# Kernel tuning notes

Measured on AMD Instinct MI355X. Metric: run time of the kernel, lower is better.

The kernel has to match this reference:

```python
import jax, jax.numpy as jnp
import numpy as np

EPS = 1e-6

def setup_inputs() -> dict:
    key = jax.random.key(0)
    k1, k2, k3 = jax.random.split(key, 3)
    B, C, H, W = 2048, 256, 7, 7
    base = jax.random.normal(k1, (B, C, H, W), dtype=jnp.float32)
    moment = jax.random.normal(k2, (B, C, H, W), dtype=jnp.float32)
    A_matrix = jax.random.randint(k3, (B, H * W, H * W), 0, 2, dtype=jnp.int32)
    return {"base": base, "moment": moment, "A_matrix": A_matrix}

def reference(base, moment, A_matrix):
    B, C, H, W = base.shape
    P = H * W  # 49
    b = base.reshape(B, C, P)      # (B, C, 49)
    m = moment.reshape(B, C, P)    # (B, C, 49)
    # pairwise dot over channel dim via batched matmul (avoids BxCx49x49 broadcast)
    dots = jnp.einsum('bcp,bcq->bpq', b, m)            # (B, 49, 49)
    nb = jnp.maximum(jnp.linalg.norm(b, axis=1), EPS)  # (B, 49)
    nm = jnp.maximum(jnp.linalg.norm(m, axis=1), EPS)  # (B, 49)
    cos_sim = dots / (nb[:, :, None] * nm[:, None, :])
    mask = A_matrix.astype(bool)
    # masked mean without dynamic-size gather
    num = jnp.sum(jnp.where(mask, cos_sim, 0.0))
    den = jnp.sum(mask).astype(cos_sim.dtype)
    return -(num / den)
```

## Files before the change

### kernel.cpp

```cpp
#include <hip/hip_runtime.h>
#include <hip/hip_bf16.h>
#include <stdint.h>


typedef __attribute__((ext_vector_type(8))) short short8;
typedef __attribute__((ext_vector_type(4))) float floatx4;

#define P 49
#define CP 12544
#define NMASK 2401
#define MT_STRIDE 264
#define WS_STRIDE 72

__device__ __forceinline__ uint16_t f2bf(float x) {
  union { float f; uint32_t u; } v; v.f = x;
  uint32_t r = v.u + 0x7fffu + ((v.u >> 16) & 1u);
  return (uint16_t)(r >> 16);
}
__device__ __forceinline__ float bf2f(uint16_t h) {
  union { uint32_t u; float f; } v; v.u = ((uint32_t)h) << 16; return v.f;
}

__device__ __forceinline__ void stage_T(const float* __restrict__ src,
                                        uint16_t* dstT, float* nred,
                                        int wv, int mrow, int kgrp) {
  float s0[8], s1[8];
  #pragma unroll
  for (int j = 0; j < 8; ++j) { s0[j] = 0.f; s1[j] = 0.f; }

  #pragma unroll
  for (int cti = 0; cti < 2; ++cti) {
    const int c = (2 * wv + cti) * 16 + mrow;
    const float* row = src + c * P;
    float4 a0 = *(const float4*)(row + kgrp * 8);
    float4 a1 = *(const float4*)(row + kgrp * 8 + 4);
    float4 b0, b1;
    if (kgrp < 2) {
      b0 = *(const float4*)(row + 32 + kgrp * 8);
      b1 = *(const float4*)(row + 32 + kgrp * 8 + 4);
    } else if (kgrp == 2) {
      b0 = make_float4(row[48], 0.f, 0.f, 0.f);
      b1 = make_float4(0.f, 0.f, 0.f, 0.f);
    } else {
      b0 = make_float4(0.f, 0.f, 0.f, 0.f);
      b1 = make_float4(0.f, 0.f, 0.f, 0.f);
    }
    s0[0] = fmaf(a0.x, a0.x, s0[0]); s0[1] = fmaf(a0.y, a0.y, s0[1]);
    s0[2] = fmaf(a0.z, a0.z, s0[2]); s0[3] = fmaf(a0.w, a0.w, s0[3]);
    s0[4] = fmaf(a1.x, a1.x, s0[4]); s0[5] = fmaf(a1.y, a1.y, s0[5]);
    s0[6] = fmaf(a1.z, a1.z, s0[6]); s0[7] = fmaf(a1.w, a1.w, s0[7]);
    s1[0] = fmaf(b0.x, b0.x, s1[0]); s1[1] = fmaf(b0.y, b0.y, s1[1]);
    s1[2] = fmaf(b0.z, b0.z, s1[2]); s1[3] = fmaf(b0.w, b0.w, s1[3]);
    s1[4] = fmaf(b1.x, b1.x, s1[4]); s1[5] = fmaf(b1.y, b1.y, s1[5]);
    s1[6] = fmaf(b1.z, b1.z, s1[6]); s1[7] = fmaf(b1.w, b1.w, s1[7]);

    float av[8] = {a0.x, a0.y, a0.z, a0.w, a1.x, a1.y, a1.z, a1.w};
    #pragma unroll
    for (int j = 0; j < 8; ++j)
      dstT[(kgrp * 8 + j) * MT_STRIDE + c] = f2bf(av[j]);
    if (kgrp < 2) {
      float bw[8] = {b0.x, b0.y, b0.z, b0.w, b1.x, b1.y, b1.z, b1.w};
      #pragma unroll
      for (int j = 0; j < 8; ++j)
        dstT[(32 + kgrp * 8 + j) * MT_STRIDE + c] = f2bf(bw[j]);
    } else if (kgrp == 2) {
      dstT[48 * MT_STRIDE + c] = f2bf(b0.x);
    }
  }

  #pragma unroll
  for (int j = 0; j < 8; ++j) {
    s0[j] += __shfl_xor(s0[j], 1); s0[j] += __shfl_xor(s0[j], 2);
    s0[j] += __shfl_xor(s0[j], 4); s0[j] += __shfl_xor(s0[j], 8);
    s1[j] += __shfl_xor(s1[j], 1); s1[j] += __shfl_xor(s1[j], 2);
    s1[j] += __shfl_xor(s1[j], 4); s1[j] += __shfl_xor(s1[j], 8);
  }
  if (mrow == 0) {
    float* nb_ = nred + wv * 64 + kgrp * 8;
    *(float4*)(nb_ + 0)  = make_float4(s0[0], s0[1], s0[2], s0[3]);
    *(float4*)(nb_ + 4)  = make_float4(s0[4], s0[5], s0[6], s0[7]);
    *(float4*)(nb_ + 32) = make_float4(s1[0], s1[1], s1[2], s1[3]);
    *(float4*)(nb_ + 36) = make_float4(s1[4], s1[5], s1[6], s1[7]);
  }
}

__global__ __launch_bounds__(512, 4) void pixpro_main(
    const float* __restrict__ base, const float* __restrict__ moment,
    const int* __restrict__ A, float* __restrict__ ws_num, float* __restrict__ ws_cnt)
{
  __shared__ __align__(16) uint16_t mT[P * MT_STRIDE];
  __shared__ __align__(16) uint16_t bT[P * MT_STRIDE];
  __shared__ __align__(16) float nredM[8 * 64];
  __shared__ __align__(16) float nredB[8 * 64];
  __shared__ __align__(16) uint16_t wS[P * WS_STRIDE];
  __shared__ float numredS[8], cntredS[8];

  const int b    = blockIdx.x;
  const int tid  = threadIdx.x;
  const int lane = tid & 63;
  const int wv   = tid >> 6;
  const int mrow = lane & 15;
  const int kgrp = (lane >> 4) & 3;

  const float* gb = base   + (size_t)b * CP;
  const float* gm = moment + (size_t)b * CP;
  const int*   gA = A      + (size_t)b * NMASK;

  stage_T(gm, mT, nredM, wv, mrow, kgrp);

  const bool btask = tid < P * 8;
  const int  bp    = tid >> 3;
  const int  bqg   = tid & 7;
  const int  bq0   = bqg * 8;
  int bmask[8];
  #pragma unroll
  for (int j = 0; j < 8; ++j) bmask[j] = 0;
  if (btask) {
    const int* Ar = gA + bp * P + bq0;
    if (bqg <= 5) {
      int4 u0 = *(const int4*)(Ar);
      int4 u1 = *(const int4*)(Ar + 4);
      bmask[0] = u0.x; bmask[1] = u0.y; bmask[2] = u0.z; bmask[3] = u0.w;
      bmask[4] = u1.x; bmask[5] = u1.y; bmask[6] = u1.z; bmask[7] = u1.w;
    } else if (bqg == 6) {
      bmask[0] = Ar[0];
    }
  }

  stage_T(gb, bT, nredB, wv, mrow, kgrp);

  __syncthreads();

  int cntpart = 0;
  if (btask) {
    float4 a0 = make_float4(0.f, 0.f, 0.f, 0.f);
    float4 a1 = make_float4(0.f, 0.f, 0.f, 0.f);
    float nb2 = 0.f;
    #pragma unroll
    for (int w = 0; w < 8; ++w) {
      const float* nr = &nredM[w * 64 + bq0];
      float4 u0 = *(const float4*)(nr);
      float4 u1 = *(const float4*)(nr + 4);
      a0.x += u0.x; a0.y += u0.y; a0.z += u0.z; a0.w += u0.w;
      a1.x += u1.x; a1.y += u1.y; a1.z += u1.z; a1.w += u1.w;
      nb2 += nredB[w * 64 + bp];
    }
    const float inb = 1.0f / fmaxf(sqrtf(nb2), 1e-6f);
    float wf[8];
    wf[0] = bmask[0] ? inb * (1.0f / fmaxf(sqrtf(a0.x), 1e-6f)) : 0.f;
    wf[1] = bmask[1] ? inb * (1.0f / fmaxf(sqrtf(a0.y), 1e-6f)) : 0.f;
    wf[2] = bmask[2] ? inb * (1.0f / fmaxf(sqrtf(a0.z), 1e-6f)) : 0.f;
    wf[3] = bmask[3] ? inb * (1.0f / fmaxf(sqrtf(a0.w), 1e-6f)) : 0.f;
    wf[4] = bmask[4] ? inb * (1.0f / fmaxf(sqrtf(a1.x), 1e-6f)) : 0.f;
    wf[5] = bmask[5] ? inb * (1.0f / fmaxf(sqrtf(a1.y), 1e-6f)) : 0.f;
    wf[6] = bmask[6] ? inb * (1.0f / fmaxf(sqrtf(a1.z), 1e-6f)) : 0.f;
    wf[7] = bmask[7] ? inb * (1.0f / fmaxf(sqrtf(a1.w), 1e-6f)) : 0.f;
    #pragma unroll
    for (int j = 0; j < 8; ++j) cntpart += bmask[j];
    short8 w8;
    #pragma unroll
    for (int j = 0; j < 8; ++j) w8[j] = (short)f2bf(wf[j]);
    *(short8*)&wS[bp * WS_STRIDE + bq0] = w8;
  }

  const int pt  = wv & 3;
  const int qt1i = 2 * (wv >> 2) + 1;
  const int pbaseV  = (pt < 3) ? pt * 16 : 33;
  const int qbase0  = (qt1i - 1) * 16;
  const int qbase1  = (qt1i < 3) ? qt1i * 16 : 33;

  const int arow  = (pbaseV + mrow) * MT_STRIDE;
  const int brow0 = (qbase0 + mrow) * MT_STRIDE;
  const int brow1 = (qbase1 + mrow) * MT_STRIDE;

  floatx4 acc0 = (floatx4){0.f, 0.f, 0.f, 0.f};
  floatx4 acc1 = (floatx4){0.f, 0.f, 0.f, 0.f};
  #pragma unroll
  for (int ks = 0; ks < 8; ++ks) {
    const int off = ks * 32 + kgrp * 8;
    short8 af  = *(const short8*)&bT[arow  + off];
    short8 bf0 = *(const short8*)&mT[brow0 + off];
    short8 bf1 = *(const short8*)&mT[brow1 + off];
    acc0 = __builtin_amdgcn_mfma_f32_16x16x32_bf16(af, bf0, acc0, 0, 0, 0);
    acc1 = __builtin_amdgcn_mfma_f32_16x16x32_bf16(af, bf1, acc1, 0, 0, 0);
  }

  __syncthreads();

  const bool vq1 = (qt1i < 3) || (mrow == 15);
  const int  q0r = qbase0 + mrow;
  const int  q1r = qbase1 + mrow;
  float numpart = 0.f;
  #pragma unroll
  for (int r = 0; r < 4; ++r) {
    const int rr = kgrp * 4 + r;
    const int p  = pbaseV + rr;
    const bool vp = (pt < 3) || (rr == 15);
    if (vp) {
      float w0 = bf2f(wS[p * WS_STRIDE + q0r]);
      float w1 = vq1 ? bf2f(wS[p * WS_STRIDE + q1r]) : 0.f;
      numpart = fmaf(w0, acc0[r], numpart);
      numpart = fmaf(w1, acc1[r], numpart);
    }
  }

  float cntf = (float)cntpart;
  #pragma unroll
  for (int off = 32; off > 0; off >>= 1) {
    numpart += __shfl_xor(numpart, off);
    cntf    += __shfl_xor(cntf, off);
  }
  if (lane == 0) { numredS[wv] = numpart; cntredS[wv] = cntf; }
  __syncthreads();

  if (tid < 64) {
    float n = (tid < 8) ? numredS[tid] : 0.f;
    float c = (tid < 8) ? cntredS[tid] : 0.f;
    #pragma unroll
    for (int off = 4; off > 0; off >>= 1) {
      n += __shfl_xor(n, off);
      c += __shfl_xor(c, off);
    }
    if (tid == 0) { ws_num[b] = n; ws_cnt[b] = c; }
  }
}

__global__ __launch_bounds__(256) void pixpro_reduce(
    const float* __restrict__ ws_num, const float* __restrict__ ws_cnt,
    float* __restrict__ out)
{
  __shared__ float rn[4], rc[4];
  float n = 0.f, c = 0.f;
  for (int i = threadIdx.x; i < 2048; i += 256) { n += ws_num[i]; c += ws_cnt[i]; }
  #pragma unroll
  for (int off = 32; off > 0; off >>= 1) {
    n += __shfl_down(n, off, 64);
    c += __shfl_down(c, off, 64);
  }
  const int wv = threadIdx.x >> 6, lane = threadIdx.x & 63;
  if (lane == 0) { rn[wv] = n; rc[wv] = c; }
  __syncthreads();
  if (threadIdx.x == 0) {
    float N = rn[0] + rn[1] + rn[2] + rn[3];
    float D = rc[0] + rc[1] + rc[2] + rc[3];
    out[0] = -(N / D);
  }
}

extern "C" void kernel_launch(void* const* d_in, const int* in_sizes, int n_in,
                              void* d_out, int out_size, void* d_ws, size_t ws_size,
                              hipStream_t stream) {
  const float* base   = (const float*)d_in[0];
  const float* moment = (const float*)d_in[1];
  const int*   A      = (const int*)d_in[2];
  float* ws_num = (float*)d_ws;
  float* ws_cnt = ws_num + 2048;
  pixpro_main<<<2048, 512, 0, stream>>>(base, moment, A, ws_num, ws_cnt);
  pixpro_reduce<<<1, 256, 0, stream>>>(ws_num, ws_cnt, (float*)d_out);
}
```

Before: 240.2 us.

## Stage inputs with flat coalesced float4 loads and LDS atomic norm accumulation

```diff
diff --git a/kernel.cpp b/kernel.cpp
--- a/kernel.cpp
+++ b/kernel.cpp
@@ -19,69 +19,6 @@
 }
 __device__ __forceinline__ float bf2f(uint16_t h) {
   union { uint32_t u; float f; } v; v.u = ((uint32_t)h) << 16; return v.f;
-}
-
-__device__ __forceinline__ void stage_T(const float* __restrict__ src,
-                                        uint16_t* dstT, float* nred,
-                                        int wv, int mrow, int kgrp) {
-  float s0[8], s1[8];
-  #pragma unroll
-  for (int j = 0; j < 8; ++j) { s0[j] = 0.f; s1[j] = 0.f; }
-
-  #pragma unroll
-  for (int cti = 0; cti < 2; ++cti) {
-    const int c = (2 * wv + cti) * 16 + mrow;
-    const float* row = src + c * P;
-    float4 a0 = *(const float4*)(row + kgrp * 8);
-    float4 a1 = *(const float4*)(row + kgrp * 8 + 4);
-    float4 b0, b1;
-    if (kgrp < 2) {
-      b0 = *(const float4*)(row + 32 + kgrp * 8);
-      b1 = *(const float4*)(row + 32 + kgrp * 8 + 4);
-    } else if (kgrp == 2) {
-      b0 = make_float4(row[48], 0.f, 0.f, 0.f);
-      b1 = make_float4(0.f, 0.f, 0.f, 0.f);
-    } else {
-      b0 = make_float4(0.f, 0.f, 0.f, 0.f);
-      b1 = make_float4(0.f, 0.f, 0.f, 0.f);
-    }
-    s0[0] = fmaf(a0.x, a0.x, s0[0]); s0[1] = fmaf(a0.y, a0.y, s0[1]);
-    s0[2] = fmaf(a0.z, a0.z, s0[2]); s0[3] = fmaf(a0.w, a0.w, s0[3]);
-    s0[4] = fmaf(a1.x, a1.x, s0[4]); s0[5] = fmaf(a1.y, a1.y, s0[5]);
-    s0[6] = fmaf(a1.z, a1.z, s0[6]); s0[7] = fmaf(a1.w, a1.w, s0[7]);
-    s1[0] = fmaf(b0.x, b0.x, s1[0]); s1[1] = fmaf(b0.y, b0.y, s1[1]);
-    s1[2] = fmaf(b0.z, b0.z, s1[2]); s1[3] = fmaf(b0.w, b0.w, s1[3]);
-    s1[4] = fmaf(b1.x, b1.x, s1[4]); s1[5] = fmaf(b1.y, b1.y, s1[5]);
-    s1[6] = fmaf(b1.z, b1.z, s1[6]); s1[7] = fmaf(b1.w, b1.w, s1[7]);
-
-    float av[8] = {a0.x, a0.y, a0.z, a0.w, a1.x, a1.y, a1.z, a1.w};
-    #pragma unroll
-    for (int j = 0; j < 8; ++j)
-      dstT[(kgrp * 8 + j) * MT_STRIDE + c] = f2bf(av[j]);
-    if (kgrp < 2) {
-      float bw[8] = {b0.x, b0.y, b0.z, b0.w, b1.x, b1.y, b1.z, b1.w};
-      #pragma unroll
-      for (int j = 0; j < 8; ++j)
-        dstT[(32 + kgrp * 8 + j) * MT_STRIDE + c] = f2bf(bw[j]);
-    } else if (kgrp == 2) {
-      dstT[48 * MT_STRIDE + c] = f2bf(b0.x);
-    }
-  }
-
-  #pragma unroll
-  for (int j = 0; j < 8; ++j) {
-    s0[j] += __shfl_xor(s0[j], 1); s0[j] += __shfl_xor(s0[j], 2);
-    s0[j] += __shfl_xor(s0[j], 4); s0[j] += __shfl_xor(s0[j], 8);
-    s1[j] += __shfl_xor(s1[j], 1); s1[j] += __shfl_xor(s1[j], 2);
-    s1[j] += __shfl_xor(s1[j], 4); s1[j] += __shfl_xor(s1[j], 8);
-  }
-  if (mrow == 0) {
-    float* nb_ = nred + wv * 64 + kgrp * 8;
-    *(float4*)(nb_ + 0)  = make_float4(s0[0], s0[1], s0[2], s0[3]);
-    *(float4*)(nb_ + 4)  = make_float4(s0[4], s0[5], s0[6], s0[7]);
-    *(float4*)(nb_ + 32) = make_float4(s1[0], s1[1], s1[2], s1[3]);
-    *(float4*)(nb_ + 36) = make_float4(s1[4], s1[5], s1[6], s1[7]);
-  }
 }
 
 __global__ __launch_bounds__(512, 4) void pixpro_main(
@@ -90,9 +27,9 @@
 {
   __shared__ __align__(16) uint16_t mT[P * MT_STRIDE];
   __shared__ __align__(16) uint16_t bT[P * MT_STRIDE];
-  __shared__ __align__(16) float nredM[8 * 64];
-  __shared__ __align__(16) float nredB[8 * 64];
   __shared__ __align__(16) uint16_t wS[P * WS_STRIDE];
+  __shared__ __align__(16) float nmA[P];
+  __shared__ __align__(16) float nbA[P];
   __shared__ float numredS[8], cntredS[8];
 
   const int b    = blockIdx.x;
@@ -106,7 +43,25 @@
   const float* gm = moment + (size_t)b * CP;
   const int*   gA = A      + (size_t)b * NMASK;
 
-  stage_T(gm, mT, nredM, wv, mrow, kgrp);
+  if (tid < P) { nmA[tid] = 0.f; nbA[tid] = 0.f; }
+  __syncthreads();
+
+  #pragma unroll
+  for (int r = 0; r < 7; ++r) {
+    const int e0 = (tid + r * 512) * 4;
+    if (e0 < CP) {
+      float4 v = *(const float4*)(gm + e0);
+      int c = (int)(((unsigned)e0 * 21401u) >> 20);
+      int q = e0 - c * 49;
+      float vals[4] = {v.x, v.y, v.z, v.w};
+      #pragma unroll
+      for (int j = 0; j < 4; ++j) {
+        atomicAdd(&nmA[q], vals[j] * vals[j]);
+        mT[q * MT_STRIDE + c] = f2bf(vals[j]);
+        if (++q == 49) { q = 0; ++c; }
+      }
+    }
+  }
 
   const bool btask = tid < P * 8;
   const int  bp    = tid >> 3;
@@ -127,47 +82,47 @@
     }
   }
 
-  stage_T(gb, bT, nredB, wv, mrow, kgrp);
+  #pragma unroll
+  for (int r = 0; r < 7; ++r) {
+    const int e0 = (tid + r * 512) * 4;
+    if (e0 < CP) {
+      float4 v = *(const float4*)(gb + e0);
+      int c = (int)(((unsigned)e0 * 21401u) >> 20);
+      int p = e0 - c * 49;
+      float vals[4] = {v.x, v.y, v.z, v.w};
+      #pragma unroll
+      for (int j = 0; j < 4; ++j) {
+        atomicAdd(&nbA[p], vals[j] * vals[j]);
+        bT[p * MT_STRIDE + c] = f2bf(vals[j]);
+        if (++p == 49) { p = 0; ++c; }
+      }
+    }
+  }
 
   __syncthreads();
 
   int cntpart = 0;
   if (btask) {
-    float4 a0 = make_float4(0.f, 0.f, 0.f, 0.f);
-    float4 a1 = make_float4(0.f, 0.f, 0.f, 0.f);
-    float nb2 = 0.f;
+    const float inb = 1.0f / fmaxf(sqrtf(nbA[bp]), 1e-6f);
+    float wf[8];
     #pragma unroll
-    for (int w = 0; w < 8; ++w) {
-      const float* nr = &nredM[w * 64 + bq0];
-      float4 u0 = *(const float4*)(nr);
-      float4 u1 = *(const float4*)(nr + 4);
-      a0.x += u0.x; a0.y += u0.y; a0.z += u0.z; a0.w += u0.w;
-      a1.x += u1.x; a1.y += u1.y; a1.z += u1.z; a1.w += u1.w;
-      nb2 += nredB[w * 64 + bp];
-    }
-    const float inb = 1.0f / fmaxf(sqrtf(nb2), 1e-6f);
-    float wf[8];
-    wf[0] = bmask[0] ? inb * (1.0f / fmaxf(sqrtf(a0.x), 1e-6f)) : 0.f;
-    wf[1] = bmask[1] ? inb * (1.0f / fmaxf(sqrtf(a0.y), 1e-6f)) : 0.f;
-    wf[2] = bmask[2] ? inb * (1.0f / fmaxf(sqrtf(a0.z), 1e-6f)) : 0.f;
-    wf[3] = bmask[3] ? inb * (1.0f / fmaxf(sqrtf(a0.w), 1e-6f)) : 0.f;
-    wf[4] = bmask[4] ? inb * (1.0f / fmaxf(sqrtf(a1.x), 1e-6f)) : 0.f;
-    wf[5] = bmask[5] ? inb * (1.0f / fmaxf(sqrtf(a1.y), 1e-6f)) : 0.f;
-    wf[6] = bmask[6] ? inb * (1.0f / fmaxf(sqrtf(a1.z), 1e-6f)) : 0.f;
-    wf[7] = bmask[7] ? inb * (1.0f / fmaxf(sqrtf(a1.w), 1e-6f)) : 0.f;
-    #pragma unroll
-    for (int j = 0; j < 8; ++j) cntpart += bmask[j];
+    for (int j = 0; j < 8; ++j) {
+      const int q = bq0 + j;
+      const float inm = (q < P) ? (1.0f / fmaxf(sqrtf(nmA[q]), 1e-6f)) : 0.f;
+      wf[j] = bmask[j] ? inb * inm : 0.f;
+      cntpart += bmask[j];
+    }
     short8 w8;
     #pragma unroll
     for (int j = 0; j < 8; ++j) w8[j] = (short)f2bf(wf[j]);
     *(short8*)&wS[bp * WS_STRIDE + bq0] = w8;
   }
 
-  const int pt  = wv & 3;
+  const int pt   = wv & 3;
   const int qt1i = 2 * (wv >> 2) + 1;
-  const int pbaseV  = (pt < 3) ? pt * 16 : 33;
-  const int qbase0  = (qt1i - 1) * 16;
-  const int qbase1  = (qt1i < 3) ? qt1i * 16 : 33;
+  const int pbaseV = (pt < 3) ? pt * 16 : 33;
+  const int qbase0 = (qt1i - 1) * 16;
+  const int qbase1 = (qt1i < 3) ? qt1i * 16 : 33;
 
   const int arow  = (pbaseV + mrow) * MT_STRIDE;
   const int brow0 = (qbase0 + mrow) * MT_STRIDE;
```

After: 438.8 us. +82.7%, slower.
